# Kernel optimization log

Hardware: AMD Instinct MI355X
Metric: run time of the kernel (lower is better)

## Reference

```python
import jax, jax.numpy as jnp
import numpy as np

N_WIN = 7      # regions per side (BiFormer nchw BRA default)
TOPK = 4       # routed regions per query region
NH = 1         # num_heads (RefNet_encoder uses num_heads=1)
EPS = 1e-5


def _resize(x, hw):
    n, c = x.shape[:2]
    # torch F.interpolate(mode='bilinear', align_corners=False)
    return jax.image.resize(x, (n, c, hw[0], hw[1]), method='bilinear', antialias=False)


def _conv1x1(x, w, b):
    return jnp.einsum('nchw,oc->nohw', x, w) + b[None, :, None, None]


def _ln2d(x, g, b):
    # LayerNorm over channel dim of NCHW
    mu = jnp.mean(x, axis=1, keepdims=True)
    var = jnp.var(x, axis=1, keepdims=True)
    return (x - mu) * jax.lax.rsqrt(var + EPS) * g[None, :, None, None] + b[None, :, None, None]


def _to_regions(t, nh):
    # (N,C,H,W) -> (N, nh, R, rs, hd) with R = n_win^2 regions, rs tokens/region
    n, c, h, w = t.shape
    hd = c // nh
    rh, rw = h // N_WIN, w // N_WIN
    t = t.reshape(n, nh, hd, N_WIN, rh, N_WIN, rw)
    return t.transpose(0, 1, 3, 5, 4, 6, 2).reshape(n, nh, N_WIN * N_WIN, rh * rw, hd)


def _from_regions(t, h, w):
    n, nh, _, _, hd = t.shape
    rh, rw = h // N_WIN, w // N_WIN
    t = t.reshape(n, nh, N_WIN, N_WIN, rh, rw, hd)
    return t.transpose(0, 1, 6, 2, 4, 3, 5).reshape(n, nh * hd, h, w)


def _dwconv(x, w, b):
    # depthwise 5x5 LePE conv, padding=2
    y = jax.lax.conv_general_dilated(x, w, (1, 1), 'SAME',
        dimension_numbers=('NCHW', 'OIHW', 'NCHW'), feature_group_count=x.shape[1])
    return y + b[None, :, None, None]


def _bra(x, mask, qkv_w, qkv_b, lepe_w, lepe_b, proj_w, proj_b):
    n, c, h, w = x.shape
    hd = c // NH
    scale = hd ** -0.5
    rh, rw = h // N_WIN, w // N_WIN
    rs = rh * rw
    R = N_WIN * N_WIN
    q, k, v = jnp.split(_conv1x1(x, qkv_w, qkv_b), 3, axis=1)
    # region-to-region routing graph on detached q/k (avg-pooled regions)
    qd = jax.lax.stop_gradient(q).reshape(n, c, N_WIN, rh, N_WIN, rw).mean(axis=(3, 5)).reshape(n, c, R)
    kd = jax.lax.stop_gradient(k).reshape(n, c, N_WIN, rh, N_WIN, rw).mean(axis=(3, 5)).reshape(n, c, R)
    a_r = jnp.einsum('ncp,ncq->npq', qd, kd)             # (n, R, R)
    idx = jax.lax.top_k(a_r, TOPK)[1]                     # (n, R, TOPK)
    # token-to-token attention within routed regions
    qr = _to_regions(q, NH)                               # (n, nh, R, rs, hd)
    kr = _to_regions(k, NH)
    vr = _to_regions(v, NH)
    gidx = idx[:, None, :, :, None, None]                 # (n,1,Rq,topk,1,1)
    kg = jnp.take_along_axis(kr[:, :, None], gidx, axis=3).reshape(n, NH, R, TOPK * rs, hd)
    vg = jnp.take_along_axis(vr[:, :, None], gidx, axis=3).reshape(n, NH, R, TOPK * rs, hd)
    attn = jnp.einsum('nhrqd,nhrkd->nhrqk', qr * scale, kg)
    # glass-mask additive bias, partitioned + gathered exactly like the keys
    mr = _to_regions(mask, 1)[..., 0]                     # (n,1,R,rs)
    mg = jnp.take_along_axis(mr[:, :, None], idx[:, None, :, :, None], axis=3)
    attn = attn + mg.reshape(n, 1, R, 1, TOPK * rs)
    attn = jax.nn.softmax(attn, axis=-1)
    out = jnp.einsum('nhrqk,nhrkd->nhrqd', attn, vg)
    out = _from_regions(out, h, w) + _dwconv(v, lepe_w, lepe_b)
    return _conv1x1(out, proj_w, proj_b)


def _block(x, mask, i, ln1_g, ln1_b, ln2_g, ln2_b, qkv_w, qkv_b, lepe_w, lepe_b,
           proj_w, proj_b, fc1_w, fc1_b, fc2_w, fc2_b):
    x = x + _bra(_ln2d(x, ln1_g[i], ln1_b[i]), mask, qkv_w[i], qkv_b[i],
                 lepe_w[i], lepe_b[i], proj_w[i], proj_b[i])
    h = jax.nn.gelu(_conv1x1(_ln2d(x, ln2_g[i], ln2_b[i]), fc1_w[i], fc1_b[i]), approximate=False)
    return x + _conv1x1(h, fc2_w[i], fc2_b[i])


def reference(exemplar0, exemplar, input1, exemplar_pre, conv0_w, conv0_b,
              ln1_g, ln1_b, ln2_g, ln2_b, qkv_w, qkv_b, lepe_w, lepe_b,
              proj_w, proj_b, fc1_w, fc1_b, fc2_w, fc2_b):
    hw = exemplar.shape[2:]
    pre_s = _resize(exemplar_pre, hw)
    feats_s = _resize(exemplar0, hw)
    img_s = _resize(input1, hw)
    x = jnp.concatenate([feats_s, exemplar, img_s], axis=1)
    hx = jax.lax.conv_general_dilated(x, conv0_w, (1, 1), 'SAME',
        dimension_numbers=('NCHW', 'OIHW', 'NCHW')) + conv0_b[None, :, None, None]
    m = (jax.nn.sigmoid(pre_s) > 0.5).astype(x.dtype)
    attn_mask = jnp.where(m == 0, jnp.float32(-100.0), jnp.float32(0.0)).astype(x.dtype)
    for i in range(4):
        hx = _block(hx, attn_mask, i, ln1_g, ln1_b, ln2_g, ln2_b, qkv_w, qkv_b,
                    lepe_w, lepe_b, proj_w, proj_b, fc1_w, fc1_b, fc2_w, fc2_b)
    return hx


def setup_inputs() -> dict:
    key = jax.random.key(0)
    ks = jax.random.split(key, 12)
    B, C, H, W = 4, 64, 112, 112
    s = 0.05
    return {
        'exemplar0': jax.random.normal(ks[0], (B, C, 224, 224), jnp.float32),
        'exemplar': jax.random.normal(ks[1], (B, C, H, W), jnp.float32),
        'input1': jax.random.normal(ks[2], (B, 3, 224, 224), jnp.float32),
        'exemplar_pre': jax.random.normal(ks[3], (B, 1, 224, 224), jnp.float32),
        'conv0_w': jax.random.normal(ks[4], (C, 2 * C + 3, 3, 3), jnp.float32) * s,
        'conv0_b': jnp.zeros((C,), jnp.float32),
        'ln1_g': jnp.ones((4, C), jnp.float32),
        'ln1_b': jnp.zeros((4, C), jnp.float32),
        'ln2_g': jnp.ones((4, C), jnp.float32),
        'ln2_b': jnp.zeros((4, C), jnp.float32),
        'qkv_w': jax.random.normal(ks[5], (4, 3 * C, C), jnp.float32) * s,
        'qkv_b': jnp.zeros((4, 3 * C), jnp.float32),
        'lepe_w': jax.random.normal(ks[6], (4, C, 1, 5, 5), jnp.float32) * s,
        'lepe_b': jnp.zeros((4, C), jnp.float32),
        'proj_w': jax.random.normal(ks[7], (4, C, C), jnp.float32) * s,
        'proj_b': jnp.zeros((4, C), jnp.float32),
        'fc1_w': jax.random.normal(ks[8], (4, 4 * C, C), jnp.float32) * s,
        'fc1_b': jnp.zeros((4, 4 * C), jnp.float32),
        'fc2_w': jax.random.normal(ks[9], (4, C, 4 * C), jnp.float32) * s,
        'fc2_b': jnp.zeros((4, C), jnp.float32),
    }
```

## Files before the change

### kernel.cpp

```cpp
#include <hip/hip_runtime.h>

#define HW 112
#define PP 12544
#define BB 4
#define RR 49
#define RS 256
#define GW 114
#define GP (GW*GW)
#define CK 160

typedef __bf16 bf16;
typedef __bf16 bf16x8 __attribute__((ext_vector_type(8)));
typedef __bf16 bf16x4 __attribute__((ext_vector_type(4)));
typedef float f32x4 __attribute__((ext_vector_type(4)));

__device__ __forceinline__ int swzg(int row, int halfcol, int rowbytes) {
  int byte = halfcol * 2;
  return row * rowbytes + (byte & ~127) + ((((byte >> 4) ^ row) & 7) * 16) + (byte & 15);
}
__device__ __forceinline__ int swz128(int row, int halfcol) { return swzg(row, halfcol, 128); }

__device__ __forceinline__ float gelu_fast(float x) {
  float y = 0.7978845608f * (x + 0.044715f * x * x * x);
  float t = __expf(-2.f * fabsf(y));
  float th = (1.f - t) / (1.f + t);
  th = copysignf(th, y);
  return 0.5f * x * (1.f + th);
}

__device__ __forceinline__ void gl_lds16(const void* g, void* l) {
  __builtin_amdgcn_global_load_lds((const __attribute__((address_space(1))) unsigned int*)g,
                                   (__attribute__((address_space(3))) unsigned int*)l, 16, 0, 0);
}
__device__ __forceinline__ void gl_lds4(const void* g, void* l) {
  __builtin_amdgcn_global_load_lds((const __attribute__((address_space(1))) unsigned int*)g,
                                   (__attribute__((address_space(3))) unsigned int*)l, 4, 0, 0);
}

__global__ __launch_bounds__(256) void k_ring(bf16* __restrict__ xct) {
  int t = blockIdx.x * 256 + threadIdx.x;
  if (t >= BB * 452 * 20) return;
  int c4 = t % 20; int rem = t / 20; int ri = rem % 452; int n = rem / 452;
  int hh, ww;
  if (ri < 114)      { hh = 0;   ww = ri; }
  else if (ri < 228) { hh = 113; ww = ri - 114; }
  else if (ri < 340) { hh = 1 + (ri - 228); ww = 0; }
  else               { hh = 1 + (ri - 340); ww = 113; }
  uint4 zz = {0, 0, 0, 0};
  *(uint4*)(xct + ((size_t)n * GP + hh * GW + ww) * CK + c4 * 8) = zz;
}

__global__ __launch_bounds__(256) void k_prep2(const float* __restrict__ ex0, const float* __restrict__ ex,
    const float* __restrict__ img, const float* __restrict__ pre,
    bf16* __restrict__ xct, float* __restrict__ maskr) {
  __shared__ bf16 sT2[64 * 168];
  int n = blockIdx.y;
  int p0 = blockIdx.x * 64;
  int tid = threadIdx.x;
  uint4 zz = {0, 0, 0, 0};
  for (int i2 = tid; i2 < 1344; i2 += 256) ((uint4*)sT2)[i2] = zz;
  __syncthreads();
  int l = tid & 63, g = tid >> 6;
  int p = p0 + l;
  int h = p / HW, w = p % HW;
  for (int c = g; c < 131; c += 4) {
    float val;
    if (c < 64) {
      const float* s = ex0 + (((size_t)(n * 64 + c)) * 224 + 2 * h) * 224 + 2 * w;
      val = 0.5f * (0.5f * (s[0] + s[224]) + 0.5f * (s[1] + s[225]));
    } else if (c < 128) {
      val = ex[((size_t)(n * 64 + (c - 64))) * PP + p];
    } else {
      const float* s = img + (((size_t)(n * 3 + (c - 128))) * 224 + 2 * h) * 224 + 2 * w;
      val = 0.5f * (0.5f * (s[0] + s[224]) + 0.5f * (s[1] + s[225]));
    }
    sT2[l * 168 + c] = (bf16)val;
  }
  if (tid < 64) {
    const float* s = pre + ((size_t)n * 224 + 2 * h) * 224 + 2 * w;
    float v = 0.5f * (0.5f * (s[0] + s[224]) + 0.5f * (s[1] + s[225]));
    int r = (h >> 4) * 7 + (w >> 4); int sIdx = (h & 15) * 16 + (w & 15);
    maskr[(n * RR + r) * RS + sIdx] = (v > 0.0f) ? 0.0f : -100.0f;
  }
  __syncthreads();
  for (int i2 = tid; i2 < 1280; i2 += 256) {
    int row = i2 / 20, ch = i2 % 20;
    int pr = p0 + row;
    int hh = pr / HW, ww = pr % HW;
    uint4 d = *(const uint4*)(sT2 + row * 168 + ch * 8);
    *(uint4*)(xct + ((size_t)n * GP + (hh + 1) * GW + ww + 1) * CK + ch * 8) = d;
  }
}

__global__ __launch_bounds__(256) void k_wt2(const float* __restrict__ w, bf16* __restrict__ wTb) {
  int t = blockIdx.x * 256 + threadIdx.x;
  if (t >= 9 * 5 * 64 * 32) return;
  int cc = t & 31; int o = (t >> 5) & 63; int ks = (t >> 11) % 5; int k = t / 10240;
  int c = ks * 32 + cc;
  wTb[t] = (bf16)((c < 131) ? w[((size_t)(o * 131) + c) * 9 + k] : 0.f);
}

__global__ __launch_bounds__(256) void k_wcvt(const float* __restrict__ s0, bf16* __restrict__ d0, int n0,
    const float* __restrict__ s1, bf16* __restrict__ d1, int n1,
    const float* __restrict__ s2, bf16* __restrict__ d2, int n2,
    const float* __restrict__ s3, bf16* __restrict__ d3, int n3) {
  int t = blockIdx.x * 256 + threadIdx.x;
  if (t < n0) { d0[t] = (bf16)s0[t]; return; }
  t -= n0;
  if (t < n1) { d1[t] = (bf16)s1[t]; return; }
  t -= n1;
  if (t < n2) { d2[t] = (bf16)s2[t]; return; }
  t -= n2;
  if (t < n3) { d3[t] = (bf16)s3[t]; }
}

__global__ __launch_bounds__(256) void k_conv0m(const bf16* __restrict__ xct, const bf16* __restrict__ wTb,
    const float* __restrict__ bias, float* __restrict__ out_t) {
  __shared__ bf16 sA[128 * 32];
  __shared__ bf16 sB[64 * 32];
  int n = blockIdx.y;
  int p0 = blockIdx.x * 128;
  int tid = threadIdx.x, lane = tid & 63, wv = tid >> 6;
  int lo = lane & 15, hi = lane >> 4;
  size_t gofsA[2];
  #pragma unroll
  for (int it = 0; it < 2; it++) {
    int idx = tid + it * 256;
    int row = idx >> 2, ch = idx & 3;
    int p = p0 + row;
    int hh = p / HW, ww = p % HW;
    gofsA[it] = ((size_t)(hh + 1) * GW + ww + 1) * (CK * 2) + ch * 16;
  }
  const char* xbase = (const char*)(xct + (size_t)n * GP * CK);
  f32x4 acc[2][4];
  #pragma unroll
  for (int mi = 0; mi < 2; mi++)
    #pragma unroll
    for (int ni = 0; ni < 4; ni++) acc[mi][ni] = (f32x4){0.f, 0.f, 0.f, 0.f};
  for (int tap = 0; tap < 9; tap++) {
    long shift = (long)((tap / 3 - 1) * GW + (tap % 3 - 1)) * (CK * 2);
    for (int ks = 0; ks < 5; ks++) {
      uint4 a0 = *(const uint4*)(xbase + gofsA[0] + shift + ks * 64);
      uint4 a1 = *(const uint4*)(xbase + gofsA[1] + shift + ks * 64);
      uint4 b0 = *(const uint4*)((const char*)wTb + ((size_t)(tap * 5 + ks) * 2048 + tid * 8) * 2);
      __syncthreads();
      *(uint4*)((char*)sA + tid * 16) = a0;
      *(uint4*)((char*)sA + (tid + 256) * 16) = a1;
      *(uint4*)((char*)sB + tid * 16) = b0;
      __syncthreads();
      bf16x8 aF[2], bF[4];
      #pragma unroll
      for (int mi = 0; mi < 2; mi++)
        aF[mi] = *(const bf16x8*)((const char*)sA + (wv * 32 + mi * 16 + lo) * 64 + hi * 16);
      #pragma unroll
      for (int ni = 0; ni < 4; ni++)
        bF[ni] = *(const bf16x8*)((const char*)sB + (ni * 16 + lo) * 64 + hi * 16);
      #pragma unroll
      for (int mi = 0; mi < 2; mi++)
        #pragma unroll
        for (int ni = 0; ni < 4; ni++)
          acc[mi][ni] = __builtin_amdgcn_mfma_f32_16x16x32_bf16(aF[mi], bF[ni], acc[mi][ni], 0, 0, 0);
    }
  }
  #pragma unroll
  for (int ni = 0; ni < 4; ni++) {
    float bv = bias[ni * 16 + lo];
    #pragma unroll
    for (int mi = 0; mi < 2; mi++) {
      #pragma unroll
      for (int r2 = 0; r2 < 4; r2++) {
        int p = p0 + wv * 32 + mi * 16 + hi * 4 + r2;
        out_t[((size_t)n * PP + p) * 64 + ni * 16 + lo] = acc[mi][ni][r2] + bv;
      }
    }
  }
}

__global__ __launch_bounds__(512) void k_qkvr(const float* __restrict__ xin, const float* __restrict__ lng,
    const float* __restrict__ lnb, const bf16* __restrict__ wb, const float* __restrict__ bias,
    bf16* __restrict__ qRo, bf16* __restrict__ kRo, bf16* __restrict__ vto, bf16* __restrict__ vTo,
    float* __restrict__ qd, float* __restrict__ kd) {
  __shared__ __align__(16) char smem[45056];
  bf16* sA = (bf16*)smem;
  bf16* sB = (bf16*)(smem + 32768);
  float* rq = (float*)(smem + 40960);
  float* rk = (float*)(smem + 43008);
  bf16* sT = (bf16*)smem;
  int r = blockIdx.x, n = blockIdx.y;
  int nr = n * RR + r;
  int rh = (r / 7) * 16, rw = (r % 7) * 16;
  int tid = threadIdx.x, lane = tid & 63, wv = tid >> 6;
  int lo = lane & 15, hi = lane >> 4;
  {
    int row = tid >> 1, part = tid & 1;
    int y = row >> 4, x = row & 15;
    const float* xp = xin + ((size_t)n * PP + (rh + y) * HW + rw + x) * 64 + part * 32;
    float v[32]; float s = 0.f, sq = 0.f;
    #pragma unroll
    for (int i = 0; i < 8; i++) {
      float4 d = *(const float4*)&xp[i * 4];
      v[i*4]=d.x; v[i*4+1]=d.y; v[i*4+2]=d.z; v[i*4+3]=d.w;
      s += d.x+d.y+d.z+d.w;
      sq += d.x*d.x+d.y*d.y+d.z*d.z+d.w*d.w;
    }
    s += __shfl_xor(s, 1, 64); sq += __shfl_xor(sq, 1, 64);
    float mu = s * (1.f/64.f);
    float rstd = rsqrtf(fmaxf(sq * (1.f/64.f) - mu*mu, 0.f) + 1e-5f);
    #pragma unroll
    for (int j2 = 0; j2 < 4; j2++) {
      bf16x8 o8;
      #pragma unroll
      for (int e = 0; e < 8; e++) {
        int c = part*32 + j2*8 + e;
        o8[e] = (bf16)((v[j2*8+e] - mu) * rstd * lng[c] + lnb[c]);
      }
      *(bf16x8*)((char*)sA + swz128(row, part*32 + j2*8)) = o8;
    }
  }
  for (int ob = 0; ob < 3; ob++) {
    {
      int oo = tid >> 3, q8 = tid & 7;
      uint4 d = *(const uint4*)(wb + (size_t)(ob * 64 + oo) * 64 + q8 * 8);
      *(uint4*)((char*)sB + swz128(oo, q8 * 8)) = d;
    }
    __syncthreads();
    f32x4 acc[2][4];
    #pragma unroll
    for (int mi = 0; mi < 2; mi++)
      #pragma unroll
      for (int ni = 0; ni < 4; ni++) acc[mi][ni] = (f32x4){0.f, 0.f, 0.f, 0.f};
    #pragma unroll
    for (int kk = 0; kk < 2; kk++) {
      bf16x8 aF[2], bF[4];
      #pragma unroll
      for (int mi = 0; mi < 2; mi++)
        aF[mi] = *(const bf16x8*)((const char*)sA + swz128(wv * 32 + mi * 16 + lo, kk * 32 + hi * 8));
      #pragma unroll
      for (int ni = 0; ni < 4; ni++)
        bF[ni] = *(const bf16x8*)((const char*)sB + swz128(ni * 16 + lo, kk * 32 + hi * 8));
      #pragma unroll
      for (int mi = 0; mi < 2; mi++)
        #pragma unroll
        for (int ni = 0; ni < 4; ni++)
          acc[mi][ni] = __builtin_amdgcn_mfma_f32_16x16x32_bf16(aF[mi], bF[ni], acc[mi][ni], 0, 0, 0);
    }
    float bv[4];
    #pragma unroll
    for (int ni = 0; ni < 4; ni++) bv[ni] = bias[ob * 64 + ni * 16 + lo];
    if (ob == 0) {
      float part_[4] = {0.f, 0.f, 0.f, 0.f};
      #pragma unroll
      for (int ni = 0; ni < 4; ni++) {
        #pragma unroll
        for (int mi = 0; mi < 2; mi++) {
          #pragma unroll
          for (int r2 = 0; r2 < 4; r2++) {
            float rv = acc[mi][ni][r2] + bv[ni];
            int s = wv * 32 + mi * 16 + hi * 4 + r2;
            qRo[((size_t)nr * RS + s) * 64 + ni * 16 + lo] = (bf16)(rv * 0.125f);
            part_[ni] += rv;
          }
        }
        part_[ni] += __shfl_xor(part_[ni], 16, 64);
        part_[ni] += __shfl_xor(part_[ni], 32, 64);
        if (hi == 0) rq[wv * 64 + ni * 16 + lo] = part_[ni];
      }
      __syncthreads();
    } else if (ob == 1) {
      float part_[4] = {0.f, 0.f, 0.f, 0.f};
      #pragma unroll
      for (int ni = 0; ni < 4; ni++) {
        #pragma unroll
        for (int mi = 0; mi < 2; mi++) {
          #pragma unroll
          for (int r2 = 0; r2 < 4; r2++) {
            float rv = acc[mi][ni][r2] + bv[ni];
            int s = wv * 32 + mi * 16 + hi * 4 + r2;
            kRo[((size_t)nr * RS + s) * 64 + ni * 16 + lo] = (bf16)rv;
            part_[ni] += rv;
          }
        }
        part_[ni] += __shfl_xor(part_[ni], 16, 64);
        part_[ni] += __shfl_xor(part_[ni], 32, 64);
        if (hi == 0) rk[wv * 64 + ni * 16 + lo] = part_[ni];
      }
      __syncthreads();
    } else {
      __syncthreads();
      #pragma unroll
      for (int ni = 0; ni < 4; ni++) {
        int ch = ni * 16 + lo;
        #pragma unroll
        for (int mi = 0; mi < 2; mi++) {
          #pragma unroll
          for (int r2 = 0; r2 < 4; r2++) {
            float rv = acc[mi][ni][r2] + bv[ni];
            int s = wv * 32 + mi * 16 + hi * 4 + r2;
            bf16 b = (bf16)rv;
            vto[((size_t)n * PP + (rh + (s >> 4)) * HW + rw + (s & 15)) * 64 + ch] = b;
            sT[ch * 264 + s] = b;
          }
        }
      }
      __syncthreads();
      #pragma unroll
      for (int it = 0; it < 4; it++) {
        int idx = tid + it * 512;
        int row = idx >> 5, ch8 = idx & 31;
        uint4 d = *(const uint4*)(sT + row * 264 + ch8 * 8);
        *(uint4*)(vTo + ((size_t)nr * 64 + row) * 256 + ch8 * 8) = d;
      }
      if (tid < 64) {
        int c = tid;
        float aq = 0.f, ak = 0.f;
        #pragma unroll
        for (int w8 = 0; w8 < 8; w8++) { aq += rq[w8 * 64 + c]; ak += rk[w8 * 64 + c]; }
        qd[(n * 64 + c) * RR + r] = aq * (1.f / 256.f);
        kd[(n * 64 + c) * RR + r] = ak * (1.f / 256.f);
      }
    }
  }
}

__global__ __launch_bounds__(64) void k_topk(const float* __restrict__ qd, const float* __restrict__ kd,
    int* __restrict__ gidx) {
  int pq = blockIdx.x, n = blockIdx.y;
  int j = threadIdx.x;
  float a = -3e38f;
  if (j < RR) {
    a = 0.f;
    for (int c = 0; c < 64; c++)
      a += qd[(n * 64 + c) * RR + pq] * kd[(n * 64 + c) * RR + j];
  }
  for (int t = 0; t < 4; t++) {
    float bv = a; int bj = j;
    #pragma unroll
    for (int d = 32; d >= 1; d >>= 1) {
      float ov = __shfl_xor(bv, d, 64);
      int oj = __shfl_xor(bj, d, 64);
      if (ov > bv || (ov == bv && oj < bj)) { bv = ov; bj = oj; }
    }
    if (j == 0) gidx[(n * RR + pq) * 4 + t] = bj;
    if (j == bj) a = -3e38f;
  }
}

__global__ __launch_bounds__(512, 6) void k_attn(const bf16* __restrict__ qR, const bf16* __restrict__ kR,
    const bf16* __restrict__ vT, const float* __restrict__ maskr, const int* __restrict__ gidx,
    bf16* __restrict__ attnRb) {
  __shared__ bf16 sKd[2][64 * 64];
  __shared__ bf16 sVd[2][64 * 64];
  __shared__ bf16 sP[8][16 * 64];
  __shared__ float sMaskB[2][64];
  int bid = blockIdx.x;
  int newid = (bid & 7) * 49 + (bid >> 3);
  int n = newid / (RR * 2); int rem = newid % (RR * 2); int r = rem >> 1, qsp = rem & 1;
  int tid = threadIdx.x, lane = tid & 63, wv = tid >> 6;
  int lo = lane & 15, hi = lane >> 4;
  int m0 = qsp * 128 + wv * 16;
  const bf16* qbase = qR + ((size_t)(n * RR + r)) * RS * 64;
  bf16x8 qF[2];
  #pragma unroll
  for (int kk = 0; kk < 2; kk++)
    qF[kk] = *(const bf16x8*)(qbase + (m0 + lo) * 64 + kk * 32 + hi * 8);

  int gofsK, gofsV;
  {
    int rowT = wv * 8 + (lane >> 3);
    int c4 = ((lane & 7) ^ rowT) & 7;
    gofsK = rowT * 128 + c4 * 16;
    gofsV = rowT * 512 + c4 * 16;
  }

  const int* gptr = gidx + (n * RR + r) * 4;
  int j0g = gptr[0], j1g = gptr[1], j2g = gptr[2], j3g = gptr[3];

  f32x4 zero4 = {0.f, 0.f, 0.f, 0.f};
  f32x4 Oacc[4];
  #pragma unroll
  for (int di = 0; di < 4; di++) Oacc[di] = zero4;
  float mrun = -3e38f, lrun = 0.f;

  #define ISSUE_TILE(JREG, SUB, BUF) do {                                            \
    const char* kb_ = (const char*)(kR + ((size_t)(n * RR + (JREG))) * RS * 64) + (SUB) * 8192; \
    const char* vb_ = (const char*)(vT + ((size_t)(n * RR + (JREG))) * 64 * RS) + (SUB) * 128;  \
    gl_lds16(kb_ + gofsK, (char*)sKd + (BUF) * 8192 + wv * 1024);                    \
    gl_lds16(vb_ + gofsV, (char*)sVd + (BUF) * 8192 + wv * 1024);                    \
    if (wv == 0) gl_lds4(maskr + ((size_t)(n * RR + (JREG))) * RS + (SUB) * 64 + lane, (char*)sMaskB[(BUF)]); \
  } while (0)

  ISSUE_TILE(j0g, 0, 0);

  for (int ts = 0; ts < 16; ts++) {
    int cur = ts & 1;
    asm volatile("s_waitcnt lgkmcnt(0)" ::: "memory");
    __builtin_amdgcn_s_barrier();
    __builtin_amdgcn_sched_barrier(0);
    if (ts < 15) {
      int nts = ts + 1;
      int jn = (nts < 8) ? (nts < 4 ? j0g : j1g) : (nts < 12 ? j2g : j3g);
      int nsub = nts & 3;
      ISSUE_TILE(jn, nsub, cur ^ 1);
      if (wv == 0) { asm volatile("s_waitcnt vmcnt(3)" ::: "memory"); }
      else         { asm volatile("s_waitcnt vmcnt(2)" ::: "memory"); }
    } else {
      asm volatile("s_waitcnt vmcnt(0)" ::: "memory");
    }
    __builtin_amdgcn_s_barrier();
    __builtin_amdgcn_sched_barrier(0);
    const char* sK = (const char*)sKd + cur * 8192;
    const char* sV = (const char*)sVd + cur * 8192;
    f32x4 Sacc[4];
    #pragma unroll
    for (int ni = 0; ni < 4; ni++) Sacc[ni] = zero4;
    #pragma unroll
    for (int kk = 0; kk < 2; kk++) {
      #pragma unroll
      for (int ni = 0; ni < 4; ni++) {
        bf16x8 kF = *(const bf16x8*)(sK + swz128(ni * 16 + lo, kk * 32 + hi * 8));
        Sacc[ni] = __builtin_amdgcn_mfma_f32_16x16x32_bf16(kF, qF[kk], Sacc[ni], 0, 0, 0);
      }
    }
    const float* mB = sMaskB[cur];
    float ml = -3e38f;
    #pragma unroll
    for (int ni = 0; ni < 4; ni++) {
      #pragma unroll
      for (int jj = 0; jj < 4; jj++) {
        float sv = Sacc[ni][jj] + mB[ni * 16 + hi * 4 + jj];
        Sacc[ni][jj] = sv;
        ml = fmaxf(ml, sv);
      }
    }
    ml = fmaxf(ml, __shfl_xor(ml, 16, 64));
    ml = fmaxf(ml, __shfl_xor(ml, 32, 64));
    float nm = fmaxf(mrun, ml);
    float sc = __expf(mrun - nm);
    float rs = 0.f;
    bf16* sPw = sP[wv];
    #pragma unroll
    for (int ni = 0; ni < 4; ni++) {
      bf16x4 p4;
      #pragma unroll
      for (int jj = 0; jj < 4; jj++) {
        float pv = __expf(Sacc[ni][jj] - nm);
        rs += pv;
        p4[jj] = (bf16)pv;
      }
      *(bf16x4*)((char*)sPw + swz128(lo, ni * 16 + hi * 4)) = p4;
    }
    rs += __shfl_xor(rs, 16, 64);
    rs += __shfl_xor(rs, 32, 64);
    mrun = nm; lrun = lrun * sc + rs;
    float scq[4];
    #pragma unroll
    for (int jj = 0; jj < 4; jj++) scq[jj] = __shfl(sc, hi * 4 + jj, 16);
    #pragma unroll
    for (int di = 0; di < 4; di++)
      #pragma unroll
      for (int jj = 0; jj < 4; jj++) Oacc[di][jj] *= scq[jj];
    #pragma unroll
    for (int kk = 0; kk < 2; kk++) {
      bf16x8 pF = *(const bf16x8*)((const char*)sPw + swz128(lo, kk * 32 + hi * 8));
      #pragma unroll
      for (int di = 0; di < 4; di++) {
        bf16x8 vF = *(const bf16x8*)(sV + swz128(di * 16 + lo, kk * 32 + hi * 8));
        Oacc[di] = __builtin_amdgcn_mfma_f32_16x16x32_bf16(pF, vF, Oacc[di], 0, 0, 0);
      }
    }
  }
  #undef ISSUE_TILE
  __syncthreads();
  float inv = 1.f / lrun;
  float invq[4];
  #pragma unroll
  for (int jj = 0; jj < 4; jj++) invq[jj] = __shfl(inv, hi * 4 + jj, 16);
  bf16* sOut = (bf16*)sKd;
  #pragma unroll
  for (int jj = 0; jj < 4; jj++) {
    int row = wv * 16 + hi * 4 + jj;
    #pragma unroll
    for (int di = 0; di < 4; di++)
      sOut[row * 64 + di * 16 + lo] = (bf16)(Oacc[di][jj] * invq[jj]);
  }
  __syncthreads();
  bf16* dst = attnRb + (((size_t)(n * RR + r)) * RS + qsp * 128) * 64;
  #pragma unroll
  for (int it = 0; it < 2; it++) {
    int idx = tid + it * 512;
    *(uint4*)(dst + idx * 8) = *(const uint4*)(sOut + idx * 8);
  }
}

__global__ __launch_bounds__(512) void k_lepe3(const bf16* __restrict__ v_t, const bf16* __restrict__ attnRb,
    const float* __restrict__ lw, const float* __restrict__ lb,
    const bf16* __restrict__ pwb, const float* __restrict__ pb, float* __restrict__ xo) {
  __shared__ __align__(16) char smem[64000];
  bf16* sH = (bf16*)smem;
  float* sW = (float*)(smem + 57600);
  bf16* zA = (bf16*)smem;
  bf16* sBp = (bf16*)(smem + 32768);
  int r = blockIdx.x, n = blockIdx.y;
  int rh = (r / 7) * 16, rw = (r % 7) * 16;
  int tid = threadIdx.x, lane = tid & 63, wv = tid >> 6;
  int lo = lane & 15, hi = lane >> 4;
  for (int i = tid; i < 1600; i += 512) { int c = i / 25, k = i % 25; sW[k * 64 + c] = lw[c * 25 + k]; }
  for (int g = tid; g < 3200; g += 512) {
    int pix = g >> 3, c4 = g & 7;
    int yy = pix / 20, xx = pix % 20;
    int hh = rh + yy - 2, ww = rw + xx - 2;
    uint4 d = {0, 0, 0, 0};
    if ((unsigned)hh < HW && (unsigned)ww < HW)
      d = *(const uint4*)(v_t + ((size_t)n * PP + hh * HW + ww) * 64 + c4 * 8);
    *(uint4*)((char*)sH + pix * 144 + c4 * 16) = d;
  }
  __syncthreads();
  int pixel = tid >> 1, part = tid & 1;
  int y = pixel >> 4, x = pixel & 15;
  float acc[32];
  const bf16* ar = attnRb + (((size_t)(n * RR + r)) * RS + pixel) * 64 + part * 32;
  #pragma unroll
  for (int c8 = 0; c8 < 4; c8++) {
    bf16x8 av = *(const bf16x8*)(ar + c8 * 8);
    #pragma unroll
    for (int j = 0; j < 8; j++) acc[c8 * 8 + j] = lb[part * 32 + c8 * 8 + j] + (float)av[j];
  }
  for (int t25 = 0; t25 < 25; t25++) {
    int dh = t25 / 5, dw = t25 % 5;
    int pix = (y + dh) * 20 + (x + dw);
    #pragma unroll
    for (int c8 = 0; c8 < 4; c8++) {
      bf16x8 hv = *(const bf16x8*)((const char*)sH + pix * 144 + (part * 4 + c8) * 16);
      #pragma unroll
      for (int j = 0; j < 8; j++) acc[c8 * 8 + j] += (float)hv[j] * sW[t25 * 64 + part * 32 + c8 * 8 + j];
    }
  }
  __syncthreads();
  #pragma unroll
  for (int i = 0; i < 4; i++) {
    bf16x8 o8;
    #pragma unroll
    for (int j = 0; j < 8; j++) o8[j] = (bf16)acc[i * 8 + j];
    *(bf16x8*)((char*)zA + swz128(pixel, part * 32 + i * 8)) = o8;
  }
  {
    int oo = tid >> 3, q8 = tid & 7;
    uint4 d = *(const uint4*)(pwb + (size_t)oo * 64 + q8 * 8);
    *(uint4*)((char*)sBp + swz128(oo, q8 * 8)) = d;
  }
  __syncthreads();
  f32x4 acc2[2][4];
  #pragma unroll
  for (int mi = 0; mi < 2; mi++)
    #pragma unroll
    for (int ni = 0; ni < 4; ni++) acc2[mi][ni] = (f32x4){0.f, 0.f, 0.f, 0.f};
  #pragma unroll
  for (int kk = 0; kk < 2; kk++) {
    bf16x8 aF[2], bF[4];
    #pragma unroll
    for (int mi = 0; mi < 2; mi++)
      aF[mi] = *(const bf16x8*)((const char*)zA + swz128(wv * 32 + mi * 16 + lo, kk * 32 + hi * 8));
    #pragma unroll
    for (int ni = 0; ni < 4; ni++)
      bF[ni] = *(const bf16x8*)((const char*)sBp + swz128(ni * 16 + lo, kk * 32 + hi * 8));
    #pragma unroll
    for (int mi = 0; mi < 2; mi++)
      #pragma unroll
      for (int ni = 0; ni < 4; ni++)
        acc2[mi][ni] = __builtin_amdgcn_mfma_f32_16x16x32_bf16(aF[mi], bF[ni], acc2[mi][ni], 0, 0, 0);
  }
  #pragma unroll
  for (int ni = 0; ni < 4; ni++) {
    float bv = pb[ni * 16 + lo];
    #pragma unroll
    for (int mi = 0; mi < 2; mi++) {
      #pragma unroll
      for (int r2 = 0; r2 < 4; r2++) {
        int s = wv * 32 + mi * 16 + hi * 4 + r2;
        int p = (rh + (s >> 4)) * HW + rw + (s & 15);
        xo[((size_t)n * PP + p) * 64 + ni * 16 + lo] += acc2[mi][ni][r2] + bv;
      }
    }
  }
}

__global__ __launch_bounds__(256) void k_mlp(const float* __restrict__ xin, const float* __restrict__ lng,
    const float* __restrict__ lnb, const bf16* __restrict__ w1b, const float* __restrict__ b1,
    const bf16* __restrict__ w2b, const float* __restrict__ b2, float* __restrict__ xo) {
  __shared__ bf16 sA[64 * 64];
  __shared__ bf16 sW[128 * 64];
  __shared__ bf16 sHh[64 * 128];
  int n = blockIdx.y;
  int p0 = blockIdx.x * 64;
  int tid = threadIdx.x, lane = tid & 63, wv = tid >> 6;
  int lo = lane & 15, hi = lane >> 4;
  {
    int row = tid >> 2, part = tid & 3;
    const float* xp = xin + ((size_t)n * PP + p0 + row) * 64 + part * 16;
    float v[16]; float s = 0.f, sq = 0.f;
    #pragma unroll
    for (int i = 0; i < 4; i++) {
      float4 d = *(const float4*)&xp[i * 4];
      v[i*4]=d.x; v[i*4+1]=d.y; v[i*4+2]=d.z; v[i*4+3]=d.w;
      s += d.x+d.y+d.z+d.w;
      sq += d.x*d.x+d.y*d.y+d.z*d.z+d.w*d.w;
    }
    s += __shfl_xor(s, 1, 64); sq += __shfl_xor(sq, 1, 64);
    s += __shfl_xor(s, 2, 64); sq += __shfl_xor(sq, 2, 64);
    float mu = s * (1.f/64.f);
    float rstd = rsqrtf(fmaxf(sq * (1.f/64.f) - mu*mu, 0.f) + 1e-5f);
    #pragma unroll
    for (int j2 = 0; j2 < 2; j2++) {
      bf16x8 o8;
      #pragma unroll
      for (int e = 0; e < 8; e++) {
        int c = part*16 + j2*8 + e;
        o8[e] = (bf16)((v[j2*8+e] - mu) * rstd * lng[c] + lnb[c]);
      }
      *(bf16x8*)((char*)sA + swz128(row, part*16 + j2*8)) = o8;
    }
  }
  f32x4 oacc[4];
  #pragma unroll
  for (int ni = 0; ni < 4; ni++) oacc[ni] = (f32x4){0.f, 0.f, 0.f, 0.f};
  for (int half = 0; half < 2; half++) {
    #pragma unroll
    for (int it = 0; it < 4; it++) {
      int idx = tid + it * 256;
      int oo = idx >> 3, q8 = idx & 7;
      uint4 d = *(const uint4*)(w1b + (size_t)(half * 128 + oo) * 64 + q8 * 8);
      *(uint4*)((char*)sW + swz128(oo, q8 * 8)) = d;
    }
    __syncthreads();
    f32x4 hacc[8];
    #pragma unroll
    for (int ni = 0; ni < 8; ni++) hacc[ni] = (f32x4){0.f, 0.f, 0.f, 0.f};
    #pragma unroll
    for (int kk = 0; kk < 2; kk++) {
      bf16x8 aF = *(const bf16x8*)((const char*)sA + swz128(wv * 16 + lo, kk * 32 + hi * 8));
      #pragma unroll
      for (int ni = 0; ni < 8; ni++) {
        bf16x8 bF = *(const bf16x8*)((const char*)sW + swz128(ni * 16 + lo, kk * 32 + hi * 8));
        hacc[ni] = __builtin_amdgcn_mfma_f32_16x16x32_bf16(aF, bF, hacc[ni], 0, 0, 0);
      }
    }
    #pragma unroll
    for (int ni = 0; ni < 8; ni++) {
      float bv = b1[half * 128 + ni * 16 + lo];
      #pragma unroll
      for (int r2 = 0; r2 < 4; r2++) {
        float hval = gelu_fast(hacc[ni][r2] + bv);
        *(bf16*)((char*)sHh + swzg(wv * 16 + hi * 4 + r2, ni * 16 + lo, 256)) = (bf16)hval;
      }
    }
    __syncthreads();
    #pragma unroll
    for (int it = 0; it < 4; it++) {
      int idx = tid + it * 256;
      int oo = idx >> 4, q8 = idx & 15;
      uint4 d = *(const uint4*)(w2b + (size_t)oo * 256 + half * 128 + q8 * 8);
      *(uint4*)((char*)sW + swzg(oo, q8 * 8, 256)) = d;
    }
    __syncthreads();
    #pragma unroll
    for (int kk = 0; kk < 4; kk++) {
      bf16x8 aH = *(const bf16x8*)((const char*)sHh + swzg(wv * 16 + lo, kk * 32 + hi * 8, 256));
      #pragma unroll
      for (int ni = 0; ni < 4; ni++) {
        bf16x8 bF = *(const bf16x8*)((const char*)sW + swzg(ni * 16 + lo, kk * 32 + hi * 8, 256));
        oacc[ni] = __builtin_amdgcn_mfma_f32_16x16x32_bf16(aH, bF, oacc[ni], 0, 0, 0);
      }
    }
    __syncthreads();
  }
  #pragma unroll
  for (int ni = 0; ni < 4; ni++) {
    float bv = b2[ni * 16 + lo];
    #pragma unroll
    for (int r2 = 0; r2 < 4; r2++) {
      int p = p0 + wv * 16 + hi * 4 + r2;
      xo[((size_t)n * PP + p) * 64 + ni * 16 + lo] += oacc[ni][r2] + bv;
    }
  }
}

__global__ __launch_bounds__(256) void k_untr(const float* __restrict__ x_t, float* __restrict__ out) {
  __shared__ float tile[64][68];
  int n = blockIdx.y; int p0 = blockIdx.x * 64;
  int tid = threadIdx.x;
  #pragma unroll
  for (int it = 0; it < 4; it++) {
    int g = tid + it * 256;
    int row = g >> 4, q = g & 15;
    float4 d = *(const float4*)&x_t[((size_t)n * PP + p0 + row) * 64 + q * 4];
    *(float4*)&tile[row][q * 4] = d;
  }
  __syncthreads();
  #pragma unroll
  for (int it = 0; it < 4; it++) {
    int g = tid + it * 256;
    int c = g >> 4, q = g & 15;
    float4 v;
    v.x = tile[q * 4 + 0][c]; v.y = tile[q * 4 + 1][c];
    v.z = tile[q * 4 + 2][c]; v.w = tile[q * 4 + 3][c];
    *(float4*)&out[((size_t)(n * 64 + c)) * PP + p0 + q * 4] = v;
  }
}

extern "C" void kernel_launch(void* const* d_in, const int* in_sizes, int n_in,
                              void* d_out, int out_size, void* d_ws, size_t ws_size,
                              hipStream_t stream) {
  const float* ex0 = (const float*)d_in[0];
  const float* ex  = (const float*)d_in[1];
  const float* img = (const float*)d_in[2];
  const float* pre = (const float*)d_in[3];
  const float* c0w = (const float*)d_in[4];
  const float* c0b = (const float*)d_in[5];
  const float* ln1g = (const float*)d_in[6];
  const float* ln1b = (const float*)d_in[7];
  const float* ln2g = (const float*)d_in[8];
  const float* ln2b = (const float*)d_in[9];
  const float* qkvw = (const float*)d_in[10];
  const float* qkvb = (const float*)d_in[11];
  const float* lw = (const float*)d_in[12];
  const float* lb = (const float*)d_in[13];
  const float* pw = (const float*)d_in[14];
  const float* pb = (const float*)d_in[15];
  const float* f1w = (const float*)d_in[16];
  const float* f1b = (const float*)d_in[17];
  const float* f2w = (const float*)d_in[18];
  const float* f2b = (const float*)d_in[19];

  float* W = (float*)d_ws;
  size_t o = 0;
  bf16* xct = (bf16*)(W + o);  o += (size_t)BB * GP * CK / 2;
  float* x_t  = W + o;         o += 3211264;
  bf16* attnRb = (bf16*)(W + o); o += 1605632;
  bf16* v_t  = (bf16*)(W + o); o += 1605632;
  bf16* qR   = (bf16*)(W + o); o += 1605632;
  bf16* kR   = (bf16*)(W + o); o += 1605632;
  bf16* vT   = (bf16*)(W + o); o += 1605632;
  float* qd = W + o;           o += 12544;
  float* kd = W + o;           o += 12544;
  float* maskr = W + o;        o += 50176;
  bf16* wTb = (bf16*)(W + o);  o += 46080;
  bf16* qkvwb = (bf16*)(W + o); o += 24576;
  bf16* pwb   = (bf16*)(W + o); o += 8192;
  bf16* f1wb  = (bf16*)(W + o); o += 32768;
  bf16* f2wb  = (bf16*)(W + o); o += 32768;
  int* gidx = (int*)(W + o);   o += 784;

  k_ring<<<dim3((BB * 452 * 20 + 255) / 256), dim3(256), 0, stream>>>(xct);
  k_prep2<<<dim3(196, BB), dim3(256), 0, stream>>>(ex0, ex, img, pre, xct, maskr);
  k_wt2<<<dim3(360), dim3(256), 0, stream>>>(c0w, wTb);
  k_wcvt<<<dim3((49152 + 16384 + 65536 + 65536 + 255) / 256), dim3(256), 0, stream>>>(
      qkvw, qkvwb, 49152, pw, pwb, 16384, f1w, f1wb, 65536, f2w, f2wb, 65536);
  k_conv0m<<<dim3(98, BB), dim3(256), 0, stream>>>(xct, wTb, c0b, x_t);
  for (int i = 0; i < 4; i++) {
    k_qkvr<<<dim3(RR, BB), dim3(512), 0, stream>>>(x_t, ln1g + i * 64, ln1b + i * 64,
        qkvwb + (size_t)i * 192 * 64, qkvb + i * 192, qR, kR, v_t, vT, qd, kd);
    k_topk<<<dim3(RR, BB), dim3(64), 0, stream>>>(qd, kd, gidx);
    k_attn<<<dim3(BB * RR * 2), dim3(512), 0, stream>>>(qR, kR, vT, maskr, gidx, attnRb);
    k_lepe3<<<dim3(RR, BB), dim3(512), 0, stream>>>(v_t, attnRb, lw + (size_t)i * 64 * 25, lb + i * 64,
        pwb + (size_t)i * 64 * 64, pb + i * 64, x_t);
    k_mlp<<<dim3(196, BB), dim3(256), 0, stream>>>(x_t, ln2g + i * 64, ln2b + i * 64,
        f1wb + (size_t)i * 256 * 64, f1b + i * 256, f2wb + (size_t)i * 64 * 256, f2b + i * 64, x_t);
  }
  k_untr<<<dim3(196, BB), dim3(256), 0, stream>>>(x_t, (float*)d_out);
}
```

Measured before the change: 474.8 us.

## Process two query row groups per wave in routed attention kernel

The attention kernel now runs 4 waves of 256 threads instead of 8 waves of 512, with each wave handling 32 query rows as two 16-row groups. Each K and V fragment read from LDS is reused for two MFMAs, which halves LDS fragment traffic per unit of work, and each thread issues twice as many global-to-LDS loads, with the vmcnt waits adjusted to match. The cost is more registers per wave and fewer waves to hide latency, and the 512-thread launch bound hint of 6 is dropped.

```diff
diff --git a/kernel.cpp b/kernel.cpp
--- a/kernel.cpp
+++ b/kernel.cpp
@@ -345,47 +345,55 @@
   }
 }
 
-__global__ __launch_bounds__(512, 6) void k_attn(const bf16* __restrict__ qR, const bf16* __restrict__ kR,
+__global__ __launch_bounds__(256) void k_attn(const bf16* __restrict__ qR, const bf16* __restrict__ kR,
     const bf16* __restrict__ vT, const float* __restrict__ maskr, const int* __restrict__ gidx,
     bf16* __restrict__ attnRb) {
   __shared__ bf16 sKd[2][64 * 64];
   __shared__ bf16 sVd[2][64 * 64];
-  __shared__ bf16 sP[8][16 * 64];
+  __shared__ bf16 sP[4][32 * 64];
   __shared__ float sMaskB[2][64];
   int bid = blockIdx.x;
   int newid = (bid & 7) * 49 + (bid >> 3);
   int n = newid / (RR * 2); int rem = newid % (RR * 2); int r = rem >> 1, qsp = rem & 1;
   int tid = threadIdx.x, lane = tid & 63, wv = tid >> 6;
   int lo = lane & 15, hi = lane >> 4;
-  int m0 = qsp * 128 + wv * 16;
+  int base = qsp * 128 + wv * 32;
   const bf16* qbase = qR + ((size_t)(n * RR + r)) * RS * 64;
-  bf16x8 qF[2];
-  #pragma unroll
-  for (int kk = 0; kk < 2; kk++)
-    qF[kk] = *(const bf16x8*)(qbase + (m0 + lo) * 64 + kk * 32 + hi * 8);
-
-  int gofsK, gofsV;
-  {
-    int rowT = wv * 8 + (lane >> 3);
+  bf16x8 qF[2][2];
+  #pragma unroll
+  for (int g = 0; g < 2; g++)
+    #pragma unroll
+    for (int kk = 0; kk < 2; kk++)
+      qF[g][kk] = *(const bf16x8*)(qbase + (base + g * 16 + lo) * 64 + kk * 32 + hi * 8);
+
+  int gofsK[2], gofsV[2];
+  #pragma unroll
+  for (int i = 0; i < 2; i++) {
+    int rowT = wv * 16 + i * 8 + (lane >> 3);
     int c4 = ((lane & 7) ^ rowT) & 7;
-    gofsK = rowT * 128 + c4 * 16;
-    gofsV = rowT * 512 + c4 * 16;
+    gofsK[i] = rowT * 128 + c4 * 16;
+    gofsV[i] = rowT * 512 + c4 * 16;
   }
 
   const int* gptr = gidx + (n * RR + r) * 4;
   int j0g = gptr[0], j1g = gptr[1], j2g = gptr[2], j3g = gptr[3];
 
   f32x4 zero4 = {0.f, 0.f, 0.f, 0.f};
-  f32x4 Oacc[4];
-  #pragma unroll
-  for (int di = 0; di < 4; di++) Oacc[di] = zero4;
-  float mrun = -3e38f, lrun = 0.f;
+  f32x4 Oacc[2][4];
+  #pragma unroll
+  for (int g = 0; g < 2; g++)
+    #pragma unroll
+    for (int di = 0; di < 4; di++) Oacc[g][di] = zero4;
+  float mrun[2] = {-3e38f, -3e38f}, lrun[2] = {0.f, 0.f};
 
   #define ISSUE_TILE(JREG, SUB, BUF) do {                                            \
     const char* kb_ = (const char*)(kR + ((size_t)(n * RR + (JREG))) * RS * 64) + (SUB) * 8192; \
     const char* vb_ = (const char*)(vT + ((size_t)(n * RR + (JREG))) * 64 * RS) + (SUB) * 128;  \
-    gl_lds16(kb_ + gofsK, (char*)sKd + (BUF) * 8192 + wv * 1024);                    \
-    gl_lds16(vb_ + gofsV, (char*)sVd + (BUF) * 8192 + wv * 1024);                    \
+    _Pragma("unroll")                                                                \
+    for (int i_ = 0; i_ < 2; i_++) {                                                 \
+      gl_lds16(kb_ + gofsK[i_], (char*)sKd + (BUF) * 8192 + wv * 2048 + i_ * 1024);  \
+      gl_lds16(vb_ + gofsV[i_], (char*)sVd + (BUF) * 8192 + wv * 2048 + i_ * 1024);  \
+    }                                                                                \
     if (wv == 0) gl_lds4(maskr + ((size_t)(n * RR + (JREG))) * RS + (SUB) * 64 + lane, (char*)sMaskB[(BUF)]); \
   } while (0)
 
@@ -401,8 +409,8 @@
       int jn = (nts < 8) ? (nts < 4 ? j0g : j1g) : (nts < 12 ? j2g : j3g);
       int nsub = nts & 3;
       ISSUE_TILE(jn, nsub, cur ^ 1);
-      if (wv == 0) { asm volatile("s_waitcnt vmcnt(3)" ::: "memory"); }
-      else         { asm volatile("s_waitcnt vmcnt(2)" ::: "memory"); }
+      if (wv == 0) { asm volatile("s_waitcnt vmcnt(5)" ::: "memory"); }
+      else         { asm volatile("s_waitcnt vmcnt(4)" ::: "memory"); }
     } else {
       asm volatile("s_waitcnt vmcnt(0)" ::: "memory");
     }
@@ -410,84 +418,104 @@
     __builtin_amdgcn_sched_barrier(0);
     const char* sK = (const char*)sKd + cur * 8192;
     const char* sV = (const char*)sVd + cur * 8192;
-    f32x4 Sacc[4];
-    #pragma unroll
-    for (int ni = 0; ni < 4; ni++) Sacc[ni] = zero4;
+    f32x4 Sacc[2][4];
+    #pragma unroll
+    for (int g = 0; g < 2; g++)
+      #pragma unroll
+      for (int ni = 0; ni < 4; ni++) Sacc[g][ni] = zero4;
     #pragma unroll
     for (int kk = 0; kk < 2; kk++) {
       #pragma unroll
       for (int ni = 0; ni < 4; ni++) {
         bf16x8 kF = *(const bf16x8*)(sK + swz128(ni * 16 + lo, kk * 32 + hi * 8));
-        Sacc[ni] = __builtin_amdgcn_mfma_f32_16x16x32_bf16(kF, qF[kk], Sacc[ni], 0, 0, 0);
+        #pragma unroll
+        for (int g = 0; g < 2; g++)
+          Sacc[g][ni] = __builtin_amdgcn_mfma_f32_16x16x32_bf16(kF, qF[g][kk], Sacc[g][ni], 0, 0, 0);
       }
     }
     const float* mB = sMaskB[cur];
-    float ml = -3e38f;
-    #pragma unroll
-    for (int ni = 0; ni < 4; ni++) {
-      #pragma unroll
-      for (int jj = 0; jj < 4; jj++) {
-        float sv = Sacc[ni][jj] + mB[ni * 16 + hi * 4 + jj];
-        Sacc[ni][jj] = sv;
-        ml = fmaxf(ml, sv);
-      }
-    }
-    ml = fmaxf(ml, __shfl_xor(ml, 16, 64));
-    ml = fmaxf(ml, __shfl_xor(ml, 32, 64));
-    float nm = fmaxf(mrun, ml);
-    float sc = __expf(mrun - nm);
-    float rs = 0.f;
     bf16* sPw = sP[wv];
-    #pragma unroll
-    for (int ni = 0; ni < 4; ni++) {
-      bf16x4 p4;
-      #pragma unroll
-      for (int jj = 0; jj < 4; jj++) {
-        float pv = __expf(Sacc[ni][jj] - nm);
-        rs += pv;
-        p4[jj] = (bf16)pv;
-      }
-      *(bf16x4*)((char*)sPw + swz128(lo, ni * 16 + hi * 4)) = p4;
-    }
-    rs += __shfl_xor(rs, 16, 64);
-    rs += __shfl_xor(rs, 32, 64);
-    mrun = nm; lrun = lrun * sc + rs;
-    float scq[4];
-    #pragma unroll
-    for (int jj = 0; jj < 4; jj++) scq[jj] = __shfl(sc, hi * 4 + jj, 16);
-    #pragma unroll
-    for (int di = 0; di < 4; di++)
-      #pragma unroll
-      for (int jj = 0; jj < 4; jj++) Oacc[di][jj] *= scq[jj];
+    float sc2[2];
+    #pragma unroll
+    for (int g = 0; g < 2; g++) {
+      float ml = -3e38f;
+      #pragma unroll
+      for (int ni = 0; ni < 4; ni++) {
+        #pragma unroll
+        for (int jj = 0; jj < 4; jj++) {
+          float sv = Sacc[g][ni][jj] + mB[ni * 16 + hi * 4 + jj];
+          Sacc[g][ni][jj] = sv;
+          ml = fmaxf(ml, sv);
+        }
+      }
+      ml = fmaxf(ml, __shfl_xor(ml, 16, 64));
+      ml = fmaxf(ml, __shfl_xor(ml, 32, 64));
+      float nm = fmaxf(mrun[g], ml);
+      float sc = __expf(mrun[g] - nm);
+      float rs = 0.f;
+      #pragma unroll
+      for (int ni = 0; ni < 4; ni++) {
+        bf16x4 p4;
+        #pragma unroll
+        for (int jj = 0; jj < 4; jj++) {
+          float pv = __expf(Sacc[g][ni][jj] - nm);
+          rs += pv;
+          p4[jj] = (bf16)pv;
+        }
+        *(bf16x4*)((char*)sPw + swz128(g * 16 + lo, ni * 16 + hi * 4)) = p4;
+      }
+      rs += __shfl_xor(rs, 16, 64);
+      rs += __shfl_xor(rs, 32, 64);
+      mrun[g] = nm; lrun[g] = lrun[g] * sc + rs;
+      sc2[g] = sc;
+    }
+    #pragma unroll
+    for (int g = 0; g < 2; g++) {
+      float scq[4];
+      #pragma unroll
+      for (int jj = 0; jj < 4; jj++) scq[jj] = __shfl(sc2[g], hi * 4 + jj, 16);
+      #pragma unroll
+      for (int di = 0; di < 4; di++)
+        #pragma unroll
+        for (int jj = 0; jj < 4; jj++) Oacc[g][di][jj] *= scq[jj];
+    }
     #pragma unroll
     for (int kk = 0; kk < 2; kk++) {
-      bf16x8 pF = *(const bf16x8*)((const char*)sPw + swz128(lo, kk * 32 + hi * 8));
+      bf16x8 pF[2];
+      #pragma unroll
+      for (int g = 0; g < 2; g++)
+        pF[g] = *(const bf16x8*)((const char*)sPw + swz128(g * 16 + lo, kk * 32 + hi * 8));
       #pragma unroll
       for (int di = 0; di < 4; di++) {
         bf16x8 vF = *(const bf16x8*)(sV + swz128(di * 16 + lo, kk * 32 + hi * 8));
-        Oacc[di] = __builtin_amdgcn_mfma_f32_16x16x32_bf16(pF, vF, Oacc[di], 0, 0, 0);
+        #pragma unroll
+        for (int g = 0; g < 2; g++)
+          Oacc[g][di] = __builtin_amdgcn_mfma_f32_16x16x32_bf16(pF[g], vF, Oacc[g][di], 0, 0, 0);
       }
     }
   }
   #undef ISSUE_TILE
   __syncthreads();
-  float inv = 1.f / lrun;
-  float invq[4];
-  #pragma unroll
-  for (int jj = 0; jj < 4; jj++) invq[jj] = __shfl(inv, hi * 4 + jj, 16);
   bf16* sOut = (bf16*)sKd;
   #pragma unroll
-  for (int jj = 0; jj < 4; jj++) {
-    int row = wv * 16 + hi * 4 + jj;
-    #pragma unroll
-    for (int di = 0; di < 4; di++)
-      sOut[row * 64 + di * 16 + lo] = (bf16)(Oacc[di][jj] * invq[jj]);
+  for (int g = 0; g < 2; g++) {
+    float inv = 1.f / lrun[g];
+    float invq[4];
+    #pragma unroll
+    for (int jj = 0; jj < 4; jj++) invq[jj] = __shfl(inv, hi * 4 + jj, 16);
+    #pragma unroll
+    for (int jj = 0; jj < 4; jj++) {
+      int row = wv * 32 + g * 16 + hi * 4 + jj;
+      #pragma unroll
+      for (int di = 0; di < 4; di++)
+        sOut[row * 64 + di * 16 + lo] = (bf16)(Oacc[g][di][jj] * invq[jj]);
+    }
   }
   __syncthreads();
   bf16* dst = attnRb + (((size_t)(n * RR + r)) * RS + qsp * 128) * 64;
   #pragma unroll
-  for (int it = 0; it < 2; it++) {
-    int idx = tid + it * 512;
+  for (int it = 0; it < 4; it++) {
+    int idx = tid + it * 256;
     *(uint4*)(dst + idx * 8) = *(const uint4*)(sOut + idx * 8);
   }
 }
@@ -760,7 +788,7 @@
     k_qkvr<<<dim3(RR, BB), dim3(512), 0, stream>>>(x_t, ln1g + i * 64, ln1b + i * 64,
         qkvwb + (size_t)i * 192 * 64, qkvb + i * 192, qR, kR, v_t, vT, qd, kd);
     k_topk<<<dim3(RR, BB), dim3(64), 0, stream>>>(qd, kd, gidx);
-    k_attn<<<dim3(BB * RR * 2), dim3(512), 0, stream>>>(qR, kR, vT, maskr, gidx, attnRb);
+    k_attn<<<dim3(BB * RR * 2), dim3(256), 0, stream>>>(qR, kR, vT, maskr, gidx, attnRb);
     k_lepe3<<<dim3(RR, BB), dim3(512), 0, stream>>>(v_t, attnRb, lw + (size_t)i * 64 * 25, lb + i * 64,
         pwb + (size_t)i * 64 * 64, pb + i * 64, x_t);
     k_mlp<<<dim3(196, BB), dim3(256), 0, stream>>>(x_t, ln2g + i * 64, ln2b + i * 64,
```

Measured after the change: 503.2 us. 1.06x slower.
